# Kernel optimization log

Hardware: AMD Instinct MI355X
Metric: run time of the kernel (lower is better)

Reference implementation:

```python
import jax, jax.numpy as jnp
import numpy as np

B, L, D, H, W = 2, 4096, 1024, 16, 128
E = D // H

def _ln(x, g, b):
    m = jnp.mean(x, axis=-1, keepdims=True)
    v = jnp.mean((x - m) ** 2, axis=-1, keepdims=True)
    return (x - m) / jnp.sqrt(v + 1e-5) * g + b

def _swa(xn, Wqkv, bqkv, Wp, bp):
    # causal sliding-window attention: query i attends keys j in [i-W+1, i]
    b_, l_, d_ = xn.shape
    nb = l_ // W
    qkv = xn @ Wqkv + bqkv
    q, k, v = jnp.split(qkv, 3, axis=-1)
    def heads(t):
        return t.reshape(b_, l_, H, E).transpose(0, 2, 1, 3)  # [B,H,L,E]
    q, k, v = heads(q), heads(k), heads(v)
    def blk(t):
        return t.reshape(b_, H, nb, W, E)
    qb, kb, vb = blk(q), blk(k), blk(v)
    # each query block sees previous block + own block (covers the W-band)
    kprev = jnp.pad(kb, ((0, 0), (0, 0), (1, 0), (0, 0), (0, 0)))[:, :, :nb]
    vprev = jnp.pad(vb, ((0, 0), (0, 0), (1, 0), (0, 0), (0, 0)))[:, :, :nb]
    kc = jnp.concatenate([kprev, kb], axis=3)  # [B,H,nb,2W,E]
    vc = jnp.concatenate([vprev, vb], axis=3)
    scores = jnp.einsum('bhnre,bhnse->bhnrs', qb, kc) / np.float32(np.sqrt(E))
    r = jnp.arange(W)[:, None]
    s = jnp.arange(2 * W)[None, :]
    band = (s >= r + 1) & (s <= r + W)          # local coords of [i-W+1, i]
    first = band & (s >= W)                     # block 0 has no previous block
    mask = jnp.concatenate([first[None], jnp.broadcast_to(band, (nb - 1, W, 2 * W))], axis=0)
    scores = jnp.where(mask[None, None], scores, jnp.float32(-1e30))
    attn = jax.nn.softmax(scores, axis=-1)
    out = jnp.einsum('bhnrs,bhnse->bhnre', attn, vc)
    out = out.reshape(b_, H, l_, E).transpose(0, 2, 1, 3).reshape(b_, l_, d_)
    return out @ Wp + bp

def _linattn(xn, Wqkv, bqkv, Wo, bo):
    # chunked recurrent form of causal linear attention (same math as cumsum version)
    b_, l_, d_ = xn.shape
    C = 128
    nc = l_ // C
    qkv = xn @ Wqkv + bqkv
    q, k, v = jnp.split(qkv, 3, axis=-1)
    q = q.reshape(b_, l_, H, E)
    k = k.reshape(b_, l_, H, E)
    v = v.reshape(b_, l_, H, E)
    q = jax.nn.elu(q * np.float32(E ** -0.5)) + np.float32(1.0001)
    k = jax.nn.elu(k) + np.float32(1.0001)
    def chunks(t):
        return t.reshape(b_, nc, C, H, E).transpose(1, 0, 3, 2, 4)  # [nc,B,H,C,E]
    qc, kc, vc = chunks(q), chunks(k), chunks(v)
    tril = jnp.tril(jnp.ones((C, C), jnp.float32))
    def step(carry, inp):
        S, z = carry
        qi, ki, vi = inp
        A = jnp.einsum('bhce,bhde->bhcd', qi, ki) * tril
        num = jnp.einsum('bhce,bhef->bhcf', qi, S) + jnp.einsum('bhcd,bhdf->bhcf', A, vi)
        den = jnp.einsum('bhce,bhe->bhc', qi, z) + A.sum(-1)
        o = num / (den[..., None] + 1e-6)
        S = S + jnp.einsum('bhce,bhcf->bhef', ki, vi)
        z = z + ki.sum(2)
        return (S, z), o
    S0 = jnp.zeros((b_, H, E, E), jnp.float32)
    z0 = jnp.zeros((b_, H, E), jnp.float32)
    _, out = jax.lax.scan(step, (S0, z0), (qc, kc, vc))
    out = out.transpose(1, 0, 3, 2, 4).reshape(b_, l_, d_)
    return out @ Wo + bo

def setup_inputs() -> dict:
    key = jax.random.key(0)
    ks = jax.random.split(key, 9)
    def w(k, shape, s=0.02):
        return jax.random.normal(k, shape, jnp.float32) * s
    return {
        'x': jax.random.normal(ks[0], (B, L, D), jnp.float32),
        'g1': jnp.ones((D,), jnp.float32), 'b1': jnp.zeros((D,), jnp.float32),
        'Wqkv_a': w(ks[1], (D, 3 * D)), 'bqkv_a': jnp.zeros((3 * D,), jnp.float32),
        'Wp_a': w(ks[2], (D, D)), 'bp_a': jnp.zeros((D,), jnp.float32),
        'Wqkv_s': w(ks[3], (D, 3 * D)), 'bqkv_s': jnp.zeros((3 * D,), jnp.float32),
        'Wo_s': w(ks[4], (D, D)), 'bo_s': jnp.zeros((D,), jnp.float32),
        'Wo': w(ks[5], (D, D)), 'bo': jnp.zeros((D,), jnp.float32),
        'gm': jnp.ones((D,), jnp.float32), 'bm': jnp.zeros((D,), jnp.float32),
        'W1': w(ks[6], (D, 4 * D)), 'b1m': jnp.zeros((4 * D,), jnp.float32),
        'W2': w(ks[7], (4 * D, D)), 'b2m': jnp.zeros((D,), jnp.float32),
    }

def reference(x, g1, b1, Wqkv_a, bqkv_a, Wp_a, bp_a, Wqkv_s, bqkv_s, Wo_s, bo_s,
              Wo, bo, gm, bm, W1, b1m, W2, b2m):
    xn = _ln(x, g1, b1)
    attn_out = _swa(xn, Wqkv_a, bqkv_a, Wp_a, bp_a)
    ssm_out = _linattn(xn, Wqkv_s, bqkv_s, Wo_s, bo_s)
    mixed = (attn_out + ssm_out) @ Wo + bo
    x1 = x + mixed
    h = _ln(x1, gm, bm)
    mlp = jax.nn.gelu(h @ W1 + b1m, approximate=False) @ W2 + b2m
    return x1 + mlp
```

## Files before the change

kernel.cpp:

```cpp
#include <hip/hip_runtime.h>
#include <hip/hip_bf16.h>
#include <math.h>

typedef __hip_bfloat16 bf16;
typedef float f32x4 __attribute__((ext_vector_type(4)));
typedef short short8 __attribute__((ext_vector_type(8)));
typedef unsigned short u16x4 __attribute__((ext_vector_type(4)));
typedef unsigned short u16x8 __attribute__((ext_vector_type(8)));

#define AS1 __attribute__((address_space(1)))
#define AS3 __attribute__((address_space(3)))

__device__ __forceinline__ void gload16(const void* g, void* l) {
  __builtin_amdgcn_global_load_lds((const AS1 unsigned int*)g, (AS3 unsigned int*)l, 16, 0, 0);
}
__device__ __forceinline__ float b2f(unsigned short u) {
  union { unsigned int i; float f; } c; c.i = ((unsigned int)u) << 16; return c.f;
}
__device__ __forceinline__ unsigned short f2b(float f) {
  bf16 h = __float2bfloat16(f);
  unsigned short s; __builtin_memcpy(&s, &h, 2); return s;
}
__device__ __forceinline__ f32x4 mfma16(short8 a, short8 b, f32x4 c) {
  return __builtin_amdgcn_mfma_f32_16x16x32_bf16(a, b, c, 0, 0, 0);
// ... 31 lines not shown
    int N, int dld, int doff) {
  __shared__ __attribute__((aligned(16))) unsigned short t[64][72];
  const int k0 = blockIdx.x * 64, n0 = blockIdx.y * 64;
  const int tid = threadIdx.x;
#pragma unroll
  for (int i = 0; i < 2; ++i) {
    int c = i * 256 + tid;
    int row = c >> 3, c8 = c & 7;
    f32x4 a = *(const f32x4*)&S[(size_t)(k0 + row) * N + n0 + c8 * 8];
    f32x4 b = *(const f32x4*)&S[(size_t)(k0 + row) * N + n0 + c8 * 8 + 4];
    u16x8 o;
#pragma unroll
    for (int j = 0; j < 4; ++j) { o[j] = f2b(a[j]); o[4 + j] = f2b(b[j]); }
    *(u16x8*)&t[row][c8 * 8] = o;
  }
  __syncthreads();
#pragma unroll
  for (int i = 0; i < 2; ++i) {
    int c = i * 256 + tid;
    int nrow = c >> 3, k8 = c & 7;
    u16x8 o;
#pragma unroll
    for (int j = 0; j < 8; ++j) o[j] = t[k8 * 8 + j][nrow];
    *(u16x8*)&D[(size_t)(n0 + nrow) * dld + doff + k0 + k8 * 8] = o;
  }
}

__global__ __launch_bounds__(256) void bias_comb(
    const float* __restrict__ a, const float* __restrict__ b, float* __restrict__ o) {
  int i = blockIdx.x * 256 + threadIdx.x;
  o[i] = a[i] + b[i];
}

#define EPI_STORE 0
#define EPI_GELU 1
#define EPI_RES 2

template <int EPI, int OF32>
__global__ __launch_bounds__(256) void gemm_bt(
    const unsigned short* __restrict__ A, const unsigned short* __restrict__ Bt,
    const float* __restrict__ bias, void* __restrict__ Cv,
    const float* __restrict__ res, int K, int ldA, int ldC) {
  __shared__ __attribute__((aligned(16))) unsigned short As[128 * 32];
  __shared__ __attribute__((aligned(16))) unsigned short Bs[128 * 32];
  const int tid = threadIdx.x, lane = tid & 63, wv = tid >> 6;
  const int wr = wv >> 1, wc = wv & 1;
  const size_t arow0 = (size_t)blockIdx.x * 128;
  const size_t brow0 = (size_t)blockIdx.y * 128;
  const int g = lane >> 4, r = lane & 15;
  f32x4 acc[4][4] = {};
  const int nK = K >> 5;
  for (int kt = 0; kt < nK; ++kt) {
    const int k0 = kt << 5;
#pragma unroll
    for (int i = 0; i < 2; ++i) {
      int chunk = (wv * 2 + i) * 64 + lane;
      int row = chunk >> 2;
      int cc = (chunk & 3) ^ (row & 3);
      gload16(&A[(arow0 + row) * ldA + k0 + cc * 8], &As[(wv * 2 + i) * 512]);
      gload16(&Bt[(brow0 + row) * (size_t)K + k0 + cc * 8], &Bs[(wv * 2 + i) * 512]);
    }
    __syncthreads();
    short8 af[4], bfr[4];
#pragma unroll
    for (int m = 0; m < 4; ++m) {
      int row = wr * 64 + m * 16 + r;
      af[m] = *(const short8*)&As[row * 32 + ((g ^ (row & 3)) * 8)];
    }
#pragma unroll
    for (int n = 0; n < 4; ++n) {
      int row = wc * 64 + n * 16 + r;
      bfr[n] = *(const short8*)&Bs[row * 32 + ((g ^ (row & 3)) * 8)];
    }
#pragma unroll
    for (int m = 0; m < 4; ++m)
#pragma unroll
      for (int n = 0; n < 4; ++n)
        acc[m][n] = mfma16(af[m], bfr[n], acc[m][n]);
    __syncthreads();
  }
#pragma unroll
  for (int m = 0; m < 4; ++m) {
#pragma unroll
    for (int n = 0; n < 4; ++n) {
      const int col = (int)brow0 + wc * 64 + n * 16 + r;
      const float bv = bias[col];
#pragma unroll
      for (int i = 0; i < 4; ++i) {
        const size_t row = arow0 + wr * 64 + m * 16 + g * 4 + i;
        float v = acc[m][n][i] + bv;
        if (EPI == EPI_GELU) v = 0.5f * v * (1.f + erff(v * 0.70710678118f));
        if (EPI == EPI_RES) v += res[row * ldC + col];
        if (OF32) ((float*)Cv)[row * ldC + col] = v;
        else ((unsigned short*)Cv)[row * ldC + col] = f2b(v);
      }
    }
  }
}

__global__ __launch_bounds__(256) void swa_kernel(
    const unsigned short* __restrict__ qkv, unsigned short* __restrict__ outc) {
  __shared__ __attribute__((aligned(16))) unsigned short Ks[256 * 64];
  __shared__ __attribute__((aligned(16))) unsigned short Vt[64 * 264];
  __shared__ __attribute__((aligned(16))) unsigned short Ps[128 * 264];
  __shared__ __attribute__((aligned(16))) float dn[128];
  const int bid = blockIdx.x;
  const int qb = bid & 31, h = (bid >> 5) & 15, b = bid >> 9;
  const long btok = (long)b * 4096;
  const long tok0 = btok + (long)qb * 128;
  const int tid = threadIdx.x, lane = tid & 63, wv = tid >> 6;
  const int g = lane >> 4, r = lane & 15;

#pragma unroll
  for (int i = 0; i < 8; ++i) {
    int chunk = (wv * 8 + i) * 64 + lane;
    int s = chunk >> 3, cc = (chunk & 7) ^ (s & 7);
    long kt = tok0 - 128 + s; if (kt < btok) kt = btok;
    gload16(&qkv[(size_t)kt * 3072 + 1024 + h * 64 + cc * 8], &Ks[(wv * 8 + i) * 512]);
  }
#pragma unroll
  for (int i = 0; i < 8; ++i) {
    int chunk = i * 256 + tid;
    int s = chunk >> 3, e8 = chunk & 7;
    long kt = tok0 - 128 + s; if (kt < btok) kt = btok;
    u16x8 u = *(const u16x8*)&qkv[(size_t)kt * 3072 + 2048 + h * 64 + e8 * 8];
#pragma unroll
    for (int j = 0; j < 8; ++j) Vt[(e8 * 8 + j) * 264 + s] = u[j];
  }
  short8 qf[2][2];
#pragma unroll
  for (int m = 0; m < 2; ++m)
#pragma unroll
    for (int kc = 0; kc < 2; ++kc)
      qf[m][kc] = *(const short8*)&qkv[(size_t)(tok0 + wv * 32 + m * 16 + r) * 3072 + h * 64 + kc * 32 + g * 8];
  __syncthreads();

  float rs[2][4] = {};
  for (int n = 0; n < 16; ++n) {
    const int srow = n * 16 + r;
    short8 kf0 = *(const short8*)&Ks[srow * 64 + ((g) ^ (srow & 7)) * 8];
    short8 kf1 = *(const short8*)&Ks[srow * 64 + ((4 + g) ^ (srow & 7)) * 8];
#pragma unroll
    for (int m = 0; m < 2; ++m) {
      f32x4 acc = {0.f, 0.f, 0.f, 0.f};
      acc = mfma16(qf[m][0], kf0, acc);
      acc = mfma16(qf[m][1], kf1, acc);
#pragma unroll
      for (int i = 0; i < 4; ++i) {
        int rr = wv * 32 + m * 16 + g * 4 + i;
        int ss = n * 16 + r;
        bool valid = (ss >= rr + 1) && (ss <= rr + 128) && (qb > 0 || ss >= 128);
        float p = valid ? __expf(acc[i] * 0.125f) : 0.f;
        rs[m][i] += p;
        Ps[rr * 264 + ss] = f2b(p);
      }
    }
  }
#pragma unroll
  for (int m = 0; m < 2; ++m)
#pragma unroll
    for (int i = 0; i < 4; ++i) {
      float v = rs[m][i];
      v += __shfl_xor(v, 1); v += __shfl_xor(v, 2);
      v += __shfl_xor(v, 4); v += __shfl_xor(v, 8);
      if (r == i) dn[wv * 32 + m * 16 + g * 4 + i] = v;
    }
  __syncthreads();
// ... 10 lines not shown
#pragma unroll
    for (int m = 0; m < 2; ++m)
#pragma unroll
      for (int n = 0; n < 4; ++n)
        oacc[m][n] = mfma16(pf[m], vf[n], oacc[m][n]);
  }
#pragma unroll
  for (int m = 0; m < 2; ++m) {
    f32x4 dv = *(const f32x4*)&dn[wv * 32 + m * 16 + g * 4];
#pragma unroll
    for (int n = 0; n < 4; ++n) {
      int col = h * 64 + n * 16 + r;
#pragma unroll
      for (int i = 0; i < 4; ++i) {
        size_t row = (size_t)(tok0 + wv * 32 + m * 16 + g * 4 + i);
        outc[row * 2048 + col] = f2b(oacc[m][n][i] / dv[i]);
      }
    }
  }
}

__global__ __launch_bounds__(256) void lin_pass1(
    const unsigned short* __restrict__ qkv, float* __restrict__ KVt, float* __restrict__ kz) {
  __shared__ __attribute__((aligned(16))) unsigned short kf[128 * 72];
  __shared__ __attribute__((aligned(16))) unsigned short vs[128 * 72];
  const int bid = blockIdx.x;
  const int ch = bid & 31, h = (bid >> 5) & 15, b = bid >> 9;
  const size_t tok0 = (size_t)b * 4096 + (size_t)ch * 128;
  const int tid = threadIdx.x;
#pragma unroll
  for (int i = 0; i < 4; ++i) {
    int c = i * 256 + tid;
    int row = c >> 3, e8 = c & 7;
    u16x8 uk = *(const u16x8*)&qkv[(tok0 + row) * 3072 + 1024 + h * 64 + e8 * 8];
    u16x8 uv = *(const u16x8*)&qkv[(tok0 + row) * 3072 + 2048 + h * 64 + e8 * 8];
    u16x8 tk;
#pragma unroll
    for (int j = 0; j < 8; ++j) {
      float x = b2f(uk[j]);
      x = (x > 0.f) ? x : expm1f(x);
      tk[j] = f2b(x + 1.0001f);
    }
    *(u16x8*)&kf[row * 72 + e8 * 8] = tk;
    *(u16x8*)&vs[row * 72 + e8 * 8] = uv;
  }
  __syncthreads();
  const int e0 = (tid & 15) * 4, f0 = (tid >> 4) * 4;
  float acc[4][4] = {};
  for (int c = 0; c < 128; ++c) {
    u16x4 ku = *(const u16x4*)&kf[c * 72 + e0];
    u16x4 vu = *(const u16x4*)&vs[c * 72 + f0];
    float ke[4], vv[4];
#pragma unroll
    for (int j = 0; j < 4; ++j) { ke[j] = b2f(ku[j]); vv[j] = b2f(vu[j]); }
#pragma unroll
    for (int jf = 0; jf < 4; ++jf)
#pragma unroll
      for (int je = 0; je < 4; ++je)
        acc[jf][je] += vv[jf] * ke[je];
  }
  const size_t base = (size_t)bid * 4096;
#pragma unroll
  for (int jf = 0; jf < 4; ++jf) {
    f32x4 o = {acc[jf][0], acc[jf][1], acc[jf][2], acc[jf][3]};
    *(f32x4*)&KVt[base + (f0 + jf) * 64 + e0] = o;
  }
  if (tid < 64) {
    float s = 0.f;
// ... 15 lines not shown
      *(f32x4*)p = run[i];
      run[i] += c;
    }
  }
  if (tid < 64) {
    float rz = 0.f;
    for (int ch = 0; ch < 32; ++ch) {
      float* p = &kz[((size_t)bh * 32 + ch) * 64 + tid];
      float c = *p; *p = rz; rz += c;
    }
  }
}

__global__ __launch_bounds__(256) void lin_pass3(
    const unsigned short* __restrict__ qkv, const float* __restrict__ KVt,
    const float* __restrict__ kz, unsigned short* __restrict__ outc) {
  __shared__ __attribute__((aligned(16))) unsigned short qf[128 * 72];
  __shared__ __attribute__((aligned(16))) unsigned short kf[128 * 72];
  __shared__ __attribute__((aligned(16))) unsigned short vt[64 * 136];
  __shared__ __attribute__((aligned(16))) unsigned short st[64 * 72];
  __shared__ __attribute__((aligned(16))) unsigned short am[128 * 136];
  __shared__ __attribute__((aligned(16))) float zs[64];
  __shared__ __attribute__((aligned(16))) float dnl[128];
  const int bid = blockIdx.x;
  const int ch = bid & 31, h = (bid >> 5) & 15, b = bid >> 9;
  const size_t tok0 = (size_t)b * 4096 + (size_t)ch * 128;
  const int tid = threadIdx.x, lane = tid & 63, wv = tid >> 6;
  const int g = lane >> 4, r = lane & 15;

#pragma unroll
  for (int i = 0; i < 4; ++i) {
    int c = i * 256 + tid;
    int row = c >> 3, e8 = c & 7;
    u16x8 uq = *(const u16x8*)&qkv[(tok0 + row) * 3072 + h * 64 + e8 * 8];
    u16x8 uk = *(const u16x8*)&qkv[(tok0 + row) * 3072 + 1024 + h * 64 + e8 * 8];
    u16x8 uv = *(const u16x8*)&qkv[(tok0 + row) * 3072 + 2048 + h * 64 + e8 * 8];
    u16x8 tq, tk;
#pragma unroll
    for (int j = 0; j < 8; ++j) {
      float x = b2f(uq[j]) * 0.125f;
      x = (x > 0.f) ? x : expm1f(x);
      tq[j] = f2b(x + 1.0001f);
      float y = b2f(uk[j]);
      y = (y > 0.f) ? y : expm1f(y);
      tk[j] = f2b(y + 1.0001f);
    }
    *(u16x8*)&qf[row * 72 + e8 * 8] = tq;
    *(u16x8*)&kf[row * 72 + e8 * 8] = tk;
#pragma unroll
    for (int j = 0; j < 8; ++j) vt[(e8 * 8 + j) * 136 + row] = uv[j];
  }
#pragma unroll
  for (int i = 0; i < 2; ++i) {
    int idx = i * 256 + tid;
    int f = idx >> 3, e8 = idx & 7;
    f32x4 s0 = *(const f32x4*)&KVt[(size_t)bid * 4096 + f * 64 + e8 * 8];
    f32x4 s1 = *(const f32x4*)&KVt[(size_t)bid * 4096 + f * 64 + e8 * 8 + 4];
    u16x8 t;
#pragma unroll
    for (int j = 0; j < 4; ++j) { t[j] = f2b(s0[j]); t[4 + j] = f2b(s1[j]); }
    *(u16x8*)&st[f * 72 + e8 * 8] = t;
  }
  if (tid < 64) zs[tid] = kz[(size_t)bid * 64 + tid];
  __syncthreads();

  short8 aq[2][2];
#pragma unroll
  for (int m = 0; m < 2; ++m)
#pragma unroll
// ... 80 lines not shown
      }
    }
  }
}

extern "C" void kernel_launch(void* const* d_in, const int* in_sizes, int n_in,
                              void* d_out, int out_size, void* d_ws, size_t ws_size,
                              hipStream_t stream) {
  (void)in_sizes; (void)n_in; (void)out_size; (void)ws_size;
  const float* x      = (const float*)d_in[0];
  const float* g1     = (const float*)d_in[1];
  const float* b1     = (const float*)d_in[2];
  const float* Wqkv_a = (const float*)d_in[3];
  const float* bqkv_a = (const float*)d_in[4];
  const float* Wp_a   = (const float*)d_in[5];
  const float* bp_a   = (const float*)d_in[6];
  const float* Wqkv_s = (const float*)d_in[7];
  const float* bqkv_s = (const float*)d_in[8];
  const float* Wo_s   = (const float*)d_in[9];
  const float* bo_s   = (const float*)d_in[10];
  const float* Wo     = (const float*)d_in[11];
  const float* bo     = (const float*)d_in[12];
  const float* gm     = (const float*)d_in[13];
  const float* bm     = (const float*)d_in[14];
  const float* W1     = (const float*)d_in[15];
  const float* b1m    = (const float*)d_in[16];
  const float* W2     = (const float*)d_in[17];
  const float* b2m    = (const float*)d_in[18];
  float* out = (float*)d_out;

  char* ws = (char*)d_ws;
  size_t off = 0;
  auto alloc = [&](size_t bytes) { char* p = ws + off; off += (bytes + 255) & ~(size_t)255; return p; };
  unsigned short* wTa   = (unsigned short*)alloc((size_t)3072 * 1024 * 2);
  unsigned short* wTs   = (unsigned short*)alloc((size_t)3072 * 1024 * 2);
  unsigned short* wTpo  = (unsigned short*)alloc((size_t)1024 * 2048 * 2);
  unsigned short* wTo   = (unsigned short*)alloc((size_t)1024 * 1024 * 2);
  unsigned short* wT1   = (unsigned short*)alloc((size_t)4096 * 1024 * 2);
  unsigned short* wT2   = (unsigned short*)alloc((size_t)1024 * 4096 * 2);
  float*          bcomb = (float*)alloc(1024 * 4);
  unsigned short* xn    = (unsigned short*)alloc((size_t)8192 * 1024 * 2);
  unsigned short* qkvA  = (unsigned short*)alloc((size_t)8192 * 3072 * 2);
  unsigned short* qkvS  = (unsigned short*)alloc((size_t)8192 * 3072 * 2);
  unsigned short* comb  = (unsigned short*)alloc((size_t)8192 * 2048 * 2);
  float*          kvt   = (float*)alloc((size_t)1024 * 4096 * 4);
  float*          kzp   = (float*)alloc((size_t)1024 * 64 * 4);
  unsigned short* gbuf  = qkvA;
  unsigned short* sum   = (unsigned short*)kvt;
  unsigned short* h_    = xn;
  float*          x1    = (float*)comb;

  transpose_w<<<dim3(16, 48), 256, 0, stream>>>(Wqkv_a, wTa, 3072, 1024, 0);
  transpose_w<<<dim3(16, 48), 256, 0, stream>>>(Wqkv_s, wTs, 3072, 1024, 0);
  transpose_w<<<dim3(16, 16), 256, 0, stream>>>(Wp_a, wTpo, 1024, 2048, 0);
  transpose_w<<<dim3(16, 16), 256, 0, stream>>>(Wo_s, wTpo, 1024, 2048, 1024);
  transpose_w<<<dim3(16, 16), 256, 0, stream>>>(Wo, wTo, 1024, 1024, 0);
  transpose_w<<<dim3(16, 64), 256, 0, stream>>>(W1, wT1, 4096, 1024, 0);
  transpose_w<<<dim3(64, 16), 256, 0, stream>>>(W2, wT2, 1024, 4096, 0);
  bias_comb<<<4, 256, 0, stream>>>(bp_a, bo_s, bcomb);

  ln_kernel<<<8192, 256, 0, stream>>>(x, g1, b1, xn);
  gemm_bt<EPI_STORE, 0><<<dim3(64, 24), 256, 0, stream>>>(xn, wTa, bqkv_a, qkvA, nullptr, 1024, 1024, 3072);
  swa_kernel<<<1024, 256, 0, stream>>>(qkvA, comb);
  gemm_bt<EPI_STORE, 0><<<dim3(64, 24), 256, 0, stream>>>(xn, wTs, bqkv_s, qkvS, nullptr, 1024, 1024, 3072);
  lin_pass1<<<1024, 256, 0, stream>>>(qkvS, kvt, kzp);
  lin_pass2<<<32, 256, 0, stream>>>(kvt, kzp);
  lin_pass3<<<1024, 256, 0, stream>>>(qkvS, kvt, kzp, comb);
  gemm_bt<EPI_STORE, 0><<<dim3(64, 8), 256, 0, stream>>>(comb, wTpo, bcomb, sum, nullptr, 2048, 2048, 1024);
  gemm_bt<EPI_RES, 1><<<dim3(64, 8), 256, 0, stream>>>(sum, wTo, bo, x1, x, 1024, 1024, 1024);
  ln_kernel<<<8192, 256, 0, stream>>>(x1, gm, bm, h_);
  gemm_bt<EPI_GELU, 0><<<dim3(64, 32), 256, 0, stream>>>(h_, wT1, b1m, gbuf, nullptr, 1024, 1024, 4096);
  gemm_bt<EPI_RES, 1><<<dim3(64, 8), 256, 0, stream>>>(gbuf, wT2, b2m, out, x1, 4096, 4096, 1024);
}
```

Baseline: 649.2 us.

## Replace GEMM with 512-thread 256-wide tiles and 4-stage pipelined global-to-LDS loads

Replaces the 128x128 single-stage GEMM with a 512-thread kernel using 256x256 or 128x256 tiles and a 4-buffer LDS ring that prefetches two K-steps ahead via direct global-to-LDS loads with explicit vmcnt waits. It adds workgroup swizzling for L2 locality and s_setprio around MFMA bursts. The aim is to hide global load latency, remove the per-iteration double __syncthreads stall and raise arithmetic intensity per tile. Larger tiles mean fewer workgroups and more LDS per block, which may limit occupancy. The per-wave LDS addressing drops the old XOR swizzle, so correctness depends on the new load mapping lining up with the fragment reads.

```diff
diff --git a/kernel.cpp b/kernel.cpp
--- a/kernel.cpp
+++ b/kernel.cpp
@@ -91,58 +91,113 @@
 #define EPI_GELU 1
 #define EPI_RES 2
 
-template <int EPI, int OF32>
-__global__ __launch_bounds__(256) void gemm_bt(
+
+#define MMQ(Q)                                                                     \
+  do {                                                                             \
+    _Pragma("unroll") for (int mm_ = 0; mm_ < 4; ++mm_) {                          \
+      _Pragma("unroll") for (int nn_ = 0; nn_ < 4; ++nn_)                          \
+          acc[(Q) * 4 + mm_][nn_] = mfma16(af[mm_], bf[nn_], acc[(Q) * 4 + mm_][nn_]); \
+    }                                                                              \
+  } while (0)
+
+#define SLOT(RR, RRS, S_)                                                          \
+  do {                                                                             \
+    const int s2_ = (S_) + 2;                                                      \
+    const bool st_ = s2_ < nS;                                                     \
+    short8 af[4], bf[4];                                                           \
+    _Pragma("unroll") for (int f_ = 0; f_ < 4; ++f_)                               \
+        af[f_] = *(const short8*)&Abuf[RR][awo + f_ * 512];                         \
+    _Pragma("unroll") for (int f_ = 0; f_ < 4; ++f_)                               \
+        bf[f_] = *(const short8*)&Bbuf[RR][bwo + f_ * 512];                         \
+    if (st_) {                                                                     \
+      gload16(gA + (size_t)s2_ * 32, &Abuf[RRS][wv * 512]);                        \
+      if constexpr (MSUB == 8) {                                                   \
+        gload16(gA + (size_t)s2_ * 32 + 128 * ldAs, &Abuf[RRS][(8 + wv) * 512]);   \
+      } else {                                                                     \
+        gload16(gB + (size_t)s2_ * 32, &Bbuf[RRS][wv * 512]);                      \
+        gload16(gB + (size_t)s2_ * 32 + 128 * Ksz, &Bbuf[RRS][(8 + wv) * 512]);    \
+      }                                                                            \
+    }                                                                              \
+    __builtin_amdgcn_s_barrier();                                                  \
+    __builtin_amdgcn_s_setprio(1);                                                 \
+    MMQ(0);                                                                        \
+    __builtin_amdgcn_s_setprio(0);                                                 \
+    if constexpr (MSUB == 8) {                                                     \
+      __builtin_amdgcn_s_barrier();                                                \
+      _Pragma("unroll") for (int f_ = 0; f_ < 4; ++f_)                             \
+          af[f_] = *(const short8*)&Abuf[RR][awo + (4 + f_) * 512];                 \
+      if (st_) {                                                                   \
+        gload16(gB + (size_t)s2_ * 32, &Bbuf[RRS][wv * 512]);                      \
+        gload16(gB + (size_t)s2_ * 32 + 128 * Ksz, &Bbuf[RRS][(8 + wv) * 512]);    \
+      }                                                                            \
+      __builtin_amdgcn_s_barrier();                                                \
+      __builtin_amdgcn_s_setprio(1);                                               \
+      MMQ(1);                                                                      \
+      __builtin_amdgcn_s_setprio(0);                                               \
+    }                                                                              \
+    if (st_) {                                                                     \
+      if constexpr (MSUB == 8) asm volatile("s_waitcnt vmcnt(4)" ::: "memory");    \
+      else asm volatile("s_waitcnt vmcnt(3)" ::: "memory");                        \
+    } else if ((S_) + 1 < nS) {                                                    \
+      asm volatile("s_waitcnt vmcnt(0)" ::: "memory");                             \
+    }                                                                              \
+    __builtin_amdgcn_s_barrier();                                                  \
+    __builtin_amdgcn_sched_barrier(0);                                             \
+  } while (0)
+
+template <int MSUB, int EPI, int OF32>
+__global__ __launch_bounds__(512, 2) void gemm8(
     const unsigned short* __restrict__ A, const unsigned short* __restrict__ Bt,
     const float* __restrict__ bias, void* __restrict__ Cv,
-    const float* __restrict__ res, int K, int ldA, int ldC) {
-  __shared__ __attribute__((aligned(16))) unsigned short As[128 * 32];
-  __shared__ __attribute__((aligned(16))) unsigned short Bs[128 * 32];
+    const float* __restrict__ res, int K, int ldA, int ldC, int lgnmt) {
+  static_assert(MSUB == 8 || MSUB == 4, "MSUB must be 8 (BM=256) or 4 (BM=128)");
+  __shared__ __attribute__((aligned(16))) unsigned short Abuf[4][MSUB * 1024];
+  __shared__ __attribute__((aligned(16))) unsigned short Bbuf[4][8192];
   const int tid = threadIdx.x, lane = tid & 63, wv = tid >> 6;
-  const int wr = wv >> 1, wc = wv & 1;
-  const size_t arow0 = (size_t)blockIdx.x * 128;
-  const size_t brow0 = (size_t)blockIdx.y * 128;
   const int g = lane >> 4, r = lane & 15;
-  f32x4 acc[4][4] = {};
-  const int nK = K >> 5;
-  for (int kt = 0; kt < nK; ++kt) {
-    const int k0 = kt << 5;
-#pragma unroll
-    for (int i = 0; i < 2; ++i) {
-      int chunk = (wv * 2 + i) * 64 + lane;
-      int row = chunk >> 2;
-      int cc = (chunk & 3) ^ (row & 3);
-      gload16(&A[(arow0 + row) * ldA + k0 + cc * 8], &As[(wv * 2 + i) * 512]);
-      gload16(&Bt[(brow0 + row) * (size_t)K + k0 + cc * 8], &Bs[(wv * 2 + i) * 512]);
-    }
-    __syncthreads();
-    short8 af[4], bfr[4];
-#pragma unroll
-    for (int m = 0; m < 4; ++m) {
-      int row = wr * 64 + m * 16 + r;
-      af[m] = *(const short8*)&As[row * 32 + ((g ^ (row & 3)) * 8)];
-    }
-#pragma unroll
-    for (int n = 0; n < 4; ++n) {
-      int row = wc * 64 + n * 16 + r;
-      bfr[n] = *(const short8*)&Bs[row * 32 + ((g ^ (row & 3)) * 8)];
-    }
-#pragma unroll
-    for (int m = 0; m < 4; ++m)
-#pragma unroll
-      for (int n = 0; n < 4; ++n)
-        acc[m][n] = mfma16(af[m], bfr[n], acc[m][n]);
-    __syncthreads();
-  }
-#pragma unroll
-  for (int m = 0; m < 4; ++m) {
+  const int wr = wv >> 2, wc = wv & 3;
+  const int bid = blockIdx.x, nwg = gridDim.x;
+  const int swz = (bid & 7) * (nwg >> 3) + (bid >> 3);
+  const int mt = swz & ((1 << lgnmt) - 1), nt = swz >> lgnmt;
+  const size_t arow0 = (size_t)mt * (MSUB * 32);
+  const size_t brow0 = (size_t)nt * 256;
+  const size_t Ksz = (size_t)K, ldAs = (size_t)ldA;
+  const unsigned short* gA = A + (arow0 + (size_t)(wv * 16 + r)) * ldAs + g * 8;
+  const unsigned short* gB = Bt + (brow0 + (size_t)(wv * 16 + r)) * Ksz + g * 8;
+  const int awo = wr * (MSUB * 512) + lane * 8;
+  const int bwo = wc * 2048 + lane * 8;
+  const int nS = K >> 5;
+  f32x4 acc[MSUB][4] = {};
+
+  gload16(gA, &Abuf[0][wv * 512]);
+  if constexpr (MSUB == 8) gload16(gA + 128 * ldAs, &Abuf[0][(8 + wv) * 512]);
+  gload16(gB, &Bbuf[0][wv * 512]);
+  gload16(gB + 128 * Ksz, &Bbuf[0][(8 + wv) * 512]);
+  gload16(gA + 32, &Abuf[1][wv * 512]);
+  if constexpr (MSUB == 8) gload16(gA + 32 + 128 * ldAs, &Abuf[1][(8 + wv) * 512]);
+  gload16(gB + 32, &Bbuf[1][wv * 512]);
+  gload16(gB + 32 + 128 * Ksz, &Bbuf[1][(8 + wv) * 512]);
+  if constexpr (MSUB == 8) asm volatile("s_waitcnt vmcnt(4)" ::: "memory");
+  else                     asm volatile("s_waitcnt vmcnt(3)" ::: "memory");
+  __builtin_amdgcn_s_barrier();
+  __builtin_amdgcn_sched_barrier(0);
+
+  for (int s4 = 0; s4 < nS; s4 += 4) {
+    SLOT(0, 2, s4 + 0);
+    SLOT(1, 3, s4 + 1);
+    SLOT(2, 0, s4 + 2);
+    SLOT(3, 1, s4 + 3);
+  }
+
+#pragma unroll
+  for (int m = 0; m < MSUB; ++m) {
 #pragma unroll
     for (int n = 0; n < 4; ++n) {
       const int col = (int)brow0 + wc * 64 + n * 16 + r;
       const float bv = bias[col];
 #pragma unroll
       for (int i = 0; i < 4; ++i) {
-        const size_t row = arow0 + wr * 64 + m * 16 + g * 4 + i;
+        const size_t row = arow0 + wr * (MSUB * 16) + m * 16 + g * 4 + i;
         float v = acc[m][n][i] + bv;
         if (EPI == EPI_GELU) v = 0.5f * v * (1.f + erff(v * 0.70710678118f));
         if (EPI == EPI_RES) v += res[row * ldC + col];
@@ -524,15 +579,15 @@
   bias_comb<<<4, 256, 0, stream>>>(bp_a, bo_s, bcomb);
 
   ln_kernel<<<8192, 256, 0, stream>>>(x, g1, b1, xn);
-  gemm_bt<EPI_STORE, 0><<<dim3(64, 24), 256, 0, stream>>>(xn, wTa, bqkv_a, qkvA, nullptr, 1024, 1024, 3072);
+  gemm8<8, EPI_STORE, 0><<<384, 512, 0, stream>>>(xn, wTa, bqkv_a, qkvA, nullptr, 1024, 1024, 3072, 5);
   swa_kernel<<<1024, 256, 0, stream>>>(qkvA, comb);
-  gemm_bt<EPI_STORE, 0><<<dim3(64, 24), 256, 0, stream>>>(xn, wTs, bqkv_s, qkvS, nullptr, 1024, 1024, 3072);
+  gemm8<8, EPI_STORE, 0><<<384, 512, 0, stream>>>(xn, wTs, bqkv_s, qkvS, nullptr, 1024, 1024, 3072, 5);
   lin_pass1<<<1024, 256, 0, stream>>>(qkvS, kvt, kzp);
   lin_pass2<<<32, 256, 0, stream>>>(kvt, kzp);
   lin_pass3<<<1024, 256, 0, stream>>>(qkvS, kvt, kzp, comb);
-  gemm_bt<EPI_STORE, 0><<<dim3(64, 8), 256, 0, stream>>>(comb, wTpo, bcomb, sum, nullptr, 2048, 2048, 1024);
-  gemm_bt<EPI_RES, 1><<<dim3(64, 8), 256, 0, stream>>>(sum, wTo, bo, x1, x, 1024, 1024, 1024);
+  gemm8<4, EPI_STORE, 0><<<256, 512, 0, stream>>>(comb, wTpo, bcomb, sum, nullptr, 2048, 2048, 1024, 6);
+  gemm8<4, EPI_RES, 1><<<256, 512, 0, stream>>>(sum, wTo, bo, x1, x, 1024, 1024, 1024, 6);
   ln_kernel<<<8192, 256, 0, stream>>>(x1, gm, bm, h_);
-  gemm_bt<EPI_GELU, 0><<<dim3(64, 32), 256, 0, stream>>>(h_, wT1, b1m, gbuf, nullptr, 1024, 1024, 4096);
-  gemm_bt<EPI_RES, 1><<<dim3(64, 8), 256, 0, stream>>>(gbuf, wT2, b2m, out, x1, 4096, 4096, 1024);
-}
+  gemm8<8, EPI_GELU, 0><<<512, 512, 0, stream>>>(h_, wT1, b1m, gbuf, nullptr, 1024, 1024, 4096, 5);
+  gemm8<4, EPI_RES, 1><<<256, 512, 0, stream>>>(gbuf, wT2, b2m, out, x1, 4096, 4096, 1024, 6);
+}
```

New measurement: 699.1 us. +7.7%, slower.

## Replace GEMM with 8-wave double-buffered ping-pong kernel using larger tiles

Applied to the files above, without the earlier changes.

Replaces the simple 128x128, K=32 single-buffered GEMM with a 512-thread kernel. It uses 256x256 (or 256x128) tiles, K=64 steps and double-buffered LDS. Global-to-LDS loads are interleaved with MFMA phases, using explicit barriers, s_setprio and vmcnt waits. A grid swizzle improves L2 locality. The aim is to hide memory latency and raise MFMA utilization across all the dense projections. The risks are higher LDS and register use, fragile hand-written synchronization, and fewer blocks for the smaller GEMMs.

```diff
diff --git a/kernel.cpp b/kernel.cpp
--- a/kernel.cpp
+++ b/kernel.cpp
@@ -91,67 +91,145 @@
 #define EPI_GELU 1
 #define EPI_RES 2
 
-template <int EPI, int OF32>
-__global__ __launch_bounds__(256) void gemm_bt(
+
+#define BAR() asm volatile("s_barrier" ::: "memory")
+#define PRIO1 __builtin_amdgcn_s_setprio(1)
+#define PRIO0 __builtin_amdgcn_s_setprio(0)
+#define VM2 asm volatile("s_waitcnt vmcnt(2)" ::: "memory")
+#define VM0 asm volatile("s_waitcnt vmcnt(0)" ::: "memory")
+
+#define RDA(CUR, MH)                                                                 \
+  _Pragma("unroll") for (int m_ = 0; m_ < 4; ++m_)                                   \
+  _Pragma("unroll") for (int ks_ = 0; ks_ < 2; ++ks_)                                \
+    a[m_][ks_] = *(const short8*)&Abuf[CUR][((wr * 8 + (MH) * 4 + m_) + 16 * ks_) * 512 + lane * 8];
+
+#define RDB(CUR, NH, BB)                                                             \
+  _Pragma("unroll") for (int n_ = 0; n_ < NQ; ++n_)                                  \
+  _Pragma("unroll") for (int ks_ = 0; ks_ < 2; ++ks_) {                              \
+    if constexpr (NQ == 2)                                                           \
+      BB[n_][ks_] = *(const short8*)&Bbuf[CUR][((wc * 4 + (NH) * 2 + n_) + 16 * ks_) * 512 + lane * 8]; \
+    else                                                                             \
+      BB[n_][ks_] = *(const short8*)&Bbuf[CUR][((wc * 2 + (NH)) + 8 * ks_) * 512 + lane * 8]; \
+  }
+
+#define MMPH(MH, NH, BB)                                                             \
+  _Pragma("unroll") for (int m_ = 0; m_ < 4; ++m_)                                   \
+  _Pragma("unroll") for (int n_ = 0; n_ < NQ; ++n_)                                  \
+  _Pragma("unroll") for (int ks_ = 0; ks_ < 2; ++ks_)                                \
+    acc[MH][NH][m_][n_] = mfma16(a[m_][ks_], BB[n_][ks_], acc[MH][NH][m_][n_]);
+
+#define STA_LO(DST, T_) do { const unsigned short* p_ = pA0 + (size_t)(T_) * 64;     \
+    gload16(p_, &Abuf[DST][wv * 512]);                                               \
+    gload16(p_ + 128 * ldAs, &Abuf[DST][(8 + wv) * 512]); } while (0)
+#define STA_HI(DST, T_) do { const unsigned short* p_ = pA0 + (size_t)(T_) * 64 + 32;\
+    gload16(p_, &Abuf[DST][(16 + wv) * 512]);                                        \
+    gload16(p_ + 128 * ldAs, &Abuf[DST][(24 + wv) * 512]); } while (0)
+#define STB_0(DST, T_) do { const unsigned short* p_ = pB0 + (size_t)(T_) * 64;      \
+    if constexpr (NQ == 2) {                                                         \
+      gload16(p_, &Bbuf[DST][wv * 512]);                                             \
+      gload16(p_ + 128 * Ksz, &Bbuf[DST][(8 + wv) * 512]);                           \
+    } else {                                                                         \
+      gload16(p_, &Bbuf[DST][wv * 512]);                                             \
+      gload16(p_ + 32, &Bbuf[DST][(8 + wv) * 512]);                                  \
+    } } while (0)
+#define STB_1(DST, T_) do { if constexpr (NQ == 2) {                                 \
+      const unsigned short* p_ = pB0 + (size_t)(T_) * 64 + 32;                       \
+      gload16(p_, &Bbuf[DST][(16 + wv) * 512]);                                      \
+      gload16(p_ + 128 * Ksz, &Bbuf[DST][(24 + wv) * 512]); } } while (0)
+
+#define TILE(CUR, T_)                                                                \
+  do {                                                                               \
+    const int Tp1_ = (T_) + 1, Tp2_ = (T_) + 2;                                      \
+    const bool s1_ = Tp1_ < nT, s2_ = Tp2_ < nT;                                     \
+                                            \
+    RDA(CUR, 0); RDB(CUR, 0, b0);                                                    \
+    if (s1_) STA_HI(CUR ^ 1, Tp1_);                                                  \
+    BAR(); PRIO1; MMPH(0, 0, b0); PRIO0; BAR();                                      \
+                                                   \
+    RDB(CUR, 1, b1);                                                                 \
+    if (s1_) STB_0(CUR ^ 1, Tp1_);                                                   \
+    BAR(); PRIO1; MMPH(0, 1, b1); PRIO0; BAR();                                      \
+                                                   \
+    RDA(CUR, 1);                                                                     \
+    if (s1_) STB_1(CUR ^ 1, Tp1_);                                                   \
+    BAR(); PRIO1; MMPH(1, 0, b0); PRIO0; BAR();                                      \
+                  \
+    if (s2_) STA_LO(CUR, Tp2_);                                                      \
+    BAR(); PRIO1; MMPH(1, 1, b1); PRIO0;                                             \
+    if (s2_) { VM2; } else { VM0; }                                                  \
+    BAR();                                                                           \
+  } while (0)
+
+template <int NQ, int EPI, int OF32>
+__global__ __launch_bounds__(512, 2) void gemm8p(
     const unsigned short* __restrict__ A, const unsigned short* __restrict__ Bt,
     const float* __restrict__ bias, void* __restrict__ Cv,
-    const float* __restrict__ res, int K, int ldA, int ldC) {
-  __shared__ __attribute__((aligned(16))) unsigned short As[128 * 32];
-  __shared__ __attribute__((aligned(16))) unsigned short Bs[128 * 32];
+    const float* __restrict__ res, int K, int ldA, int ldC, int lgnmt) {
+  __shared__ __attribute__((aligned(16))) unsigned short Abuf[2][256 * 64];
+  __shared__ __attribute__((aligned(16))) unsigned short Bbuf[2][NQ * 128 * 64];
   const int tid = threadIdx.x, lane = tid & 63, wv = tid >> 6;
-  const int wr = wv >> 1, wc = wv & 1;
-  const size_t arow0 = (size_t)blockIdx.x * 128;
-  const size_t brow0 = (size_t)blockIdx.y * 128;
   const int g = lane >> 4, r = lane & 15;
-  f32x4 acc[4][4] = {};
-  const int nK = K >> 5;
-  for (int kt = 0; kt < nK; ++kt) {
-    const int k0 = kt << 5;
-#pragma unroll
-    for (int i = 0; i < 2; ++i) {
-      int chunk = (wv * 2 + i) * 64 + lane;
-      int row = chunk >> 2;
-      int cc = (chunk & 3) ^ (row & 3);
-      gload16(&A[(arow0 + row) * ldA + k0 + cc * 8], &As[(wv * 2 + i) * 512]);
-      gload16(&Bt[(brow0 + row) * (size_t)K + k0 + cc * 8], &Bs[(wv * 2 + i) * 512]);
-    }
-    __syncthreads();
-    short8 af[4], bfr[4];
+  const int wr = wv >> 2, wc = wv & 3;
+  const int bid = blockIdx.x, nwg = gridDim.x;
+  const int swz = (bid & 7) * (nwg >> 3) + (bid >> 3);
+  const int mt = swz & ((1 << lgnmt) - 1), nt = swz >> lgnmt;
+  const size_t arow0 = (size_t)mt * 256;
+  const size_t brow0 = (size_t)nt * (NQ * 128);
+  const size_t ldAs = (size_t)ldA, Ksz = (size_t)K;
+  const unsigned short* pA0 = A + (arow0 + (size_t)(wv * 16 + r)) * ldAs + g * 8;
+  const unsigned short* pB0 = Bt + (brow0 + (size_t)(wv * 16 + r)) * Ksz + g * 8;
+  const int nT = K >> 6;
+  short8 a[4][2], b0[NQ][2], b1[NQ][2];
+  f32x4 acc[2][2][4][NQ] = {};
+
+  STA_LO(0, 0); STA_HI(0, 0); STB_0(0, 0); STB_1(0, 0);
+  STA_LO(1, 1);
+  VM2;
+  BAR();
+
+  for (int T = 0; T < nT; T += 2) {
+    TILE(0, T);
+    TILE(1, T + 1);
+  }
+
+#pragma unroll
+  for (int mh = 0; mh < 2; ++mh) {
 #pragma unroll
     for (int m = 0; m < 4; ++m) {
-      int row = wr * 64 + m * 16 + r;
-      af[m] = *(const short8*)&As[row * 32 + ((g ^ (row & 3)) * 8)];
-    }
-#pragma unroll
-    for (int n = 0; n < 4; ++n) {
-      int row = wc * 64 + n * 16 + r;
-      bfr[n] = *(const short8*)&Bs[row * 32 + ((g ^ (row & 3)) * 8)];
-    }
-#pragma unroll
-    for (int m = 0; m < 4; ++m)
-#pragma unroll
-      for (int n = 0; n < 4; ++n)
-        acc[m][n] = mfma16(af[m], bfr[n], acc[m][n]);
-    __syncthreads();
-  }
-#pragma unroll
-  for (int m = 0; m < 4; ++m) {
-#pragma unroll
-    for (int n = 0; n < 4; ++n) {
-      const int col = (int)brow0 + wc * 64 + n * 16 + r;
-      const float bv = bias[col];
-#pragma unroll
-      for (int i = 0; i < 4; ++i) {
-        const size_t row = arow0 + wr * 64 + m * 16 + g * 4 + i;
-        float v = acc[m][n][i] + bv;
-        if (EPI == EPI_GELU) v = 0.5f * v * (1.f + erff(v * 0.70710678118f));
-        if (EPI == EPI_RES) v += res[row * ldC + col];
-        if (OF32) ((float*)Cv)[row * ldC + col] = v;
-        else ((unsigned short*)Cv)[row * ldC + col] = f2b(v);
+#pragma unroll
+      for (int nh = 0; nh < 2; ++nh) {
+#pragma unroll
+        for (int n = 0; n < NQ; ++n) {
+          const int col = (int)brow0 + wc * (32 * NQ) + nh * (16 * NQ) + n * 16 + r;
+          const float bv = bias[col];
+#pragma unroll
+          for (int i = 0; i < 4; ++i) {
+            const size_t row = arow0 + wr * 128 + mh * 64 + m * 16 + g * 4 + i;
+            float v = acc[mh][nh][m][n][i] + bv;
+            if (EPI == EPI_GELU) v = 0.5f * v * (1.f + erff(v * 0.70710678118f));
+            if (EPI == EPI_RES) v += res[row * ldC + col];
+            if (OF32) ((float*)Cv)[row * ldC + col] = v;
+            else ((unsigned short*)Cv)[row * ldC + col] = f2b(v);
+          }
+        }
       }
     }
   }
 }
+
+#undef TILE
+#undef STA_LO
+#undef STA_HI
+#undef STB_0
+#undef STB_1
+#undef RDA
+#undef RDB
+#undef MMPH
+#undef BAR
+#undef PRIO1
+#undef PRIO0
+#undef VM2
+#undef VM0
 
 __global__ __launch_bounds__(256) void swa_kernel(
     const unsigned short* __restrict__ qkv, unsigned short* __restrict__ outc) {
@@ -524,15 +602,15 @@
   bias_comb<<<4, 256, 0, stream>>>(bp_a, bo_s, bcomb);
 
   ln_kernel<<<8192, 256, 0, stream>>>(x, g1, b1, xn);
-  gemm_bt<EPI_STORE, 0><<<dim3(64, 24), 256, 0, stream>>>(xn, wTa, bqkv_a, qkvA, nullptr, 1024, 1024, 3072);
+  gemm8p<2, EPI_STORE, 0><<<384, 512, 0, stream>>>(xn, wTa, bqkv_a, qkvA, nullptr, 1024, 1024, 3072, 5);
   swa_kernel<<<1024, 256, 0, stream>>>(qkvA, comb);
-  gemm_bt<EPI_STORE, 0><<<dim3(64, 24), 256, 0, stream>>>(xn, wTs, bqkv_s, qkvS, nullptr, 1024, 1024, 3072);
+  gemm8p<2, EPI_STORE, 0><<<384, 512, 0, stream>>>(xn, wTs, bqkv_s, qkvS, nullptr, 1024, 1024, 3072, 5);
   lin_pass1<<<1024, 256, 0, stream>>>(qkvS, kvt, kzp);
   lin_pass2<<<32, 256, 0, stream>>>(kvt, kzp);
   lin_pass3<<<1024, 256, 0, stream>>>(qkvS, kvt, kzp, comb);
-  gemm_bt<EPI_STORE, 0><<<dim3(64, 8), 256, 0, stream>>>(comb, wTpo, bcomb, sum, nullptr, 2048, 2048, 1024);
-  gemm_bt<EPI_RES, 1><<<dim3(64, 8), 256, 0, stream>>>(sum, wTo, bo, x1, x, 1024, 1024, 1024);
+  gemm8p<1, EPI_STORE, 0><<<256, 512, 0, stream>>>(comb, wTpo, bcomb, sum, nullptr, 2048, 2048, 1024, 5);
+  gemm8p<1, EPI_RES, 1><<<256, 512, 0, stream>>>(sum, wTo, bo, x1, x, 1024, 1024, 1024, 5);
   ln_kernel<<<8192, 256, 0, stream>>>(x1, gm, bm, h_);
-  gemm_bt<EPI_GELU, 0><<<dim3(64, 32), 256, 0, stream>>>(h_, wT1, b1m, gbuf, nullptr, 1024, 1024, 4096);
-  gemm_bt<EPI_RES, 1><<<dim3(64, 8), 256, 0, stream>>>(gbuf, wT2, b2m, out, x1, 4096, 4096, 1024);
-}
+  gemm8p<2, EPI_GELU, 0><<<512, 512, 0, stream>>>(h_, wT1, b1m, gbuf, nullptr, 1024, 1024, 4096, 5);
+  gemm8p<1, EPI_RES, 1><<<256, 512, 0, stream>>>(gbuf, wT2, b2m, out, x1, 4096, 4096, 1024, 5);
+}
```

Result: slower. 753.4 us (+16.1%).

## Double-buffer GEMM with larger tiles and merge both QKV projections

Applied to the files above, without the earlier changes.

Replaces the single-buffered 128x128 GEMM with a 512-thread double-buffered kernel that prefetches the next K-slice while running MFMAs on the current one. It uses 128x256 or 64x256 tiles, a swizzled block order for L2 reuse, and raises priority around the MFMA loop. The two QKV projections are fused into a single N=6144 GEMM with a concatenated bias and interleaved output, and all downstream readers are updated to the new row stride. Registers per thread go up, and the LDS layout drops the XOR swizzle, so bank conflicts are a risk.

```diff
diff --git a/kernel.cpp b/kernel.cpp
--- a/kernel.cpp
+++ b/kernel.cpp
@@ -87,62 +87,81 @@
   o[i] = a[i] + b[i];
 }
 
+__global__ __launch_bounds__(256) void bias_cat(
+    const float* __restrict__ a, const float* __restrict__ b, float* __restrict__ o, int N) {
+  int i = blockIdx.x * 256 + threadIdx.x;
+  o[i] = (i < N) ? a[i] : b[i - N];
+}
+
 #define EPI_STORE 0
 #define EPI_GELU 1
 #define EPI_RES 2
 
-template <int EPI, int OF32>
-__global__ __launch_bounds__(256) void gemm_bt(
+template <int TM, int EPI, int OF32>
+__global__ __launch_bounds__(512, 4) void gemm2p(
     const unsigned short* __restrict__ A, const unsigned short* __restrict__ Bt,
     const float* __restrict__ bias, void* __restrict__ Cv,
-    const float* __restrict__ res, int K, int ldA, int ldC) {
-  __shared__ __attribute__((aligned(16))) unsigned short As[128 * 32];
-  __shared__ __attribute__((aligned(16))) unsigned short Bs[128 * 32];
+    const float* __restrict__ res, int K, int ldA, int ldC, int lgnmt) {
+  __shared__ __attribute__((aligned(16))) unsigned short Ab[2][TM * 4 * 512];
+  __shared__ __attribute__((aligned(16))) unsigned short Bb[2][16 * 512];
   const int tid = threadIdx.x, lane = tid & 63, wv = tid >> 6;
-  const int wr = wv >> 1, wc = wv & 1;
-  const size_t arow0 = (size_t)blockIdx.x * 128;
-  const size_t brow0 = (size_t)blockIdx.y * 128;
   const int g = lane >> 4, r = lane & 15;
-  f32x4 acc[4][4] = {};
-  const int nK = K >> 5;
-  for (int kt = 0; kt < nK; ++kt) {
-    const int k0 = kt << 5;
-#pragma unroll
-    for (int i = 0; i < 2; ++i) {
-      int chunk = (wv * 2 + i) * 64 + lane;
-      int row = chunk >> 2;
-      int cc = (chunk & 3) ^ (row & 3);
-      gload16(&A[(arow0 + row) * ldA + k0 + cc * 8], &As[(wv * 2 + i) * 512]);
-      gload16(&Bt[(brow0 + row) * (size_t)K + k0 + cc * 8], &Bs[(wv * 2 + i) * 512]);
-    }
-    __syncthreads();
-    short8 af[4], bfr[4];
-#pragma unroll
-    for (int m = 0; m < 4; ++m) {
-      int row = wr * 64 + m * 16 + r;
-      af[m] = *(const short8*)&As[row * 32 + ((g ^ (row & 3)) * 8)];
-    }
-#pragma unroll
-    for (int n = 0; n < 4; ++n) {
-      int row = wc * 64 + n * 16 + r;
-      bfr[n] = *(const short8*)&Bs[row * 32 + ((g ^ (row & 3)) * 8)];
-    }
-#pragma unroll
-    for (int m = 0; m < 4; ++m)
+  const int wr = wv >> 2, wc = wv & 3;
+  const int bid = blockIdx.x, nwg = gridDim.x;
+  const int swz = (bid & 7) * (nwg >> 3) + (bid >> 3);
+  const int mt = swz & ((1 << lgnmt) - 1), nt = swz >> lgnmt;
+  const size_t arow0 = (size_t)mt * (TM * 64);
+  const size_t brow0 = (size_t)nt * 256;
+  const size_t ldAs = (size_t)ldA, Ksz = (size_t)K;
+  const int aw = wv & (TM * 4 - 1);
+  const unsigned short* gA = A + (arow0 + (size_t)(aw * 16 + r)) * ldAs + g * 8;
+  const unsigned short* gB0 = Bt + (brow0 + (size_t)(wv * 16 + r)) * Ksz + g * 8;
+  const unsigned short* gB1 = gB0 + 128 * Ksz;
+  const int nS = K >> 5;
+  f32x4 acc[TM * 2][4] = {};
+
+  if (TM == 2 || wv < 4) gload16(gA, &Ab[0][aw * 512]);
+  gload16(gB0, &Bb[0][wv * 512]);
+  gload16(gB1, &Bb[0][(8 + wv) * 512]);
+  asm volatile("s_waitcnt vmcnt(0)" ::: "memory");
+  __builtin_amdgcn_s_barrier();
+
+  for (int s = 0; s < nS; ++s) {
+    const int cur = s & 1;
+    if (s + 1 < nS) {
+      const size_t ko = (size_t)(s + 1) * 32;
+      if (TM == 2 || wv < 4) gload16(gA + ko, &Ab[cur ^ 1][aw * 512]);
+      gload16(gB0 + ko, &Bb[cur ^ 1][wv * 512]);
+      gload16(gB1 + ko, &Bb[cur ^ 1][(8 + wv) * 512]);
+    }
+    short8 af[TM * 2], bfr[4];
+#pragma unroll
+    for (int m = 0; m < TM * 2; ++m)
+      af[m] = *(const short8*)&Ab[cur][(wr * (TM * 2) + m) * 512 + lane * 8];
+#pragma unroll
+    for (int n = 0; n < 4; ++n)
+      bfr[n] = *(const short8*)&Bb[cur][(wc * 4 + n) * 512 + lane * 8];
+    __builtin_amdgcn_s_setprio(1);
+#pragma unroll
+    for (int m = 0; m < TM * 2; ++m)
 #pragma unroll
       for (int n = 0; n < 4; ++n)
         acc[m][n] = mfma16(af[m], bfr[n], acc[m][n]);
-    __syncthreads();
-  }
-#pragma unroll
-  for (int m = 0; m < 4; ++m) {
+    __builtin_amdgcn_s_setprio(0);
+    asm volatile("s_waitcnt vmcnt(0)" ::: "memory");
+    __builtin_amdgcn_s_barrier();
+    __builtin_amdgcn_sched_barrier(0);
+  }
+
+#pragma unroll
+  for (int m = 0; m < TM * 2; ++m) {
 #pragma unroll
     for (int n = 0; n < 4; ++n) {
       const int col = (int)brow0 + wc * 64 + n * 16 + r;
       const float bv = bias[col];
 #pragma unroll
       for (int i = 0; i < 4; ++i) {
-        const size_t row = arow0 + wr * 64 + m * 16 + g * 4 + i;
+        const size_t row = arow0 + wr * (TM * 32) + m * 16 + g * 4 + i;
         float v = acc[m][n][i] + bv;
         if (EPI == EPI_GELU) v = 0.5f * v * (1.f + erff(v * 0.70710678118f));
         if (EPI == EPI_RES) v += res[row * ldC + col];
@@ -171,14 +190,14 @@
     int chunk = (wv * 8 + i) * 64 + lane;
     int s = chunk >> 3, cc = (chunk & 7) ^ (s & 7);
     long kt = tok0 - 128 + s; if (kt < btok) kt = btok;
-    gload16(&qkv[(size_t)kt * 3072 + 1024 + h * 64 + cc * 8], &Ks[(wv * 8 + i) * 512]);
+    gload16(&qkv[(size_t)kt * 6144 + 1024 + h * 64 + cc * 8], &Ks[(wv * 8 + i) * 512]);
   }
 #pragma unroll
   for (int i = 0; i < 8; ++i) {
     int chunk = i * 256 + tid;
     int s = chunk >> 3, e8 = chunk & 7;
     long kt = tok0 - 128 + s; if (kt < btok) kt = btok;
-    u16x8 u = *(const u16x8*)&qkv[(size_t)kt * 3072 + 2048 + h * 64 + e8 * 8];
+    u16x8 u = *(const u16x8*)&qkv[(size_t)kt * 6144 + 2048 + h * 64 + e8 * 8];
 #pragma unroll
     for (int j = 0; j < 8; ++j) Vt[(e8 * 8 + j) * 264 + s] = u[j];
   }
@@ -187,7 +206,7 @@
   for (int m = 0; m < 2; ++m)
 #pragma unroll
     for (int kc = 0; kc < 2; ++kc)
-      qf[m][kc] = *(const short8*)&qkv[(size_t)(tok0 + wv * 32 + m * 16 + r) * 3072 + h * 64 + kc * 32 + g * 8];
+      qf[m][kc] = *(const short8*)&qkv[(size_t)(tok0 + wv * 32 + m * 16 + r) * 6144 + h * 64 + kc * 32 + g * 8];
   __syncthreads();
 
   float rs[2][4] = {};
@@ -264,8 +283,8 @@
   for (int i = 0; i < 4; ++i) {
     int c = i * 256 + tid;
     int row = c >> 3, e8 = c & 7;
-    u16x8 uk = *(const u16x8*)&qkv[(tok0 + row) * 3072 + 1024 + h * 64 + e8 * 8];
-    u16x8 uv = *(const u16x8*)&qkv[(tok0 + row) * 3072 + 2048 + h * 64 + e8 * 8];
+    u16x8 uk = *(const u16x8*)&qkv[(tok0 + row) * 6144 + 1024 + h * 64 + e8 * 8];
+    u16x8 uv = *(const u16x8*)&qkv[(tok0 + row) * 6144 + 2048 + h * 64 + e8 * 8];
     u16x8 tk;
 #pragma unroll
     for (int j = 0; j < 8; ++j) {
@@ -347,9 +366,9 @@
   for (int i = 0; i < 4; ++i) {
     int c = i * 256 + tid;
     int row = c >> 3, e8 = c & 7;
-    u16x8 uq = *(const u16x8*)&qkv[(tok0 + row) * 3072 + h * 64 + e8 * 8];
-    u16x8 uk = *(const u16x8*)&qkv[(tok0 + row) * 3072 + 1024 + h * 64 + e8 * 8];
-    u16x8 uv = *(const u16x8*)&qkv[(tok0 + row) * 3072 + 2048 + h * 64 + e8 * 8];
+    u16x8 uq = *(const u16x8*)&qkv[(tok0 + row) * 6144 + h * 64 + e8 * 8];
+    u16x8 uk = *(const u16x8*)&qkv[(tok0 + row) * 6144 + 1024 + h * 64 + e8 * 8];
+    u16x8 uv = *(const u16x8*)&qkv[(tok0 + row) * 6144 + 2048 + h * 64 + e8 * 8];
     u16x8 tq, tk;
 #pragma unroll
     for (int j = 0; j < 8; ++j) {
@@ -496,43 +515,42 @@
   char* ws = (char*)d_ws;
   size_t off = 0;
   auto alloc = [&](size_t bytes) { char* p = ws + off; off += (bytes + 255) & ~(size_t)255; return p; };
-  unsigned short* wTa   = (unsigned short*)alloc((size_t)3072 * 1024 * 2);
-  unsigned short* wTs   = (unsigned short*)alloc((size_t)3072 * 1024 * 2);
+  unsigned short* wTaS  = (unsigned short*)alloc((size_t)6144 * 1024 * 2);
   unsigned short* wTpo  = (unsigned short*)alloc((size_t)1024 * 2048 * 2);
   unsigned short* wTo   = (unsigned short*)alloc((size_t)1024 * 1024 * 2);
   unsigned short* wT1   = (unsigned short*)alloc((size_t)4096 * 1024 * 2);
   unsigned short* wT2   = (unsigned short*)alloc((size_t)1024 * 4096 * 2);
   float*          bcomb = (float*)alloc(1024 * 4);
+  float*          bcat  = (float*)alloc(6144 * 4);
   unsigned short* xn    = (unsigned short*)alloc((size_t)8192 * 1024 * 2);
-  unsigned short* qkvA  = (unsigned short*)alloc((size_t)8192 * 3072 * 2);
-  unsigned short* qkvS  = (unsigned short*)alloc((size_t)8192 * 3072 * 2);
+  unsigned short* qkvAS = (unsigned short*)alloc((size_t)8192 * 6144 * 2);
   unsigned short* comb  = (unsigned short*)alloc((size_t)8192 * 2048 * 2);
   float*          kvt   = (float*)alloc((size_t)1024 * 4096 * 4);
   float*          kzp   = (float*)alloc((size_t)1024 * 64 * 4);
-  unsigned short* gbuf  = qkvA;
+  unsigned short* gbuf  = qkvAS;
   unsigned short* sum   = (unsigned short*)kvt;
   unsigned short* h_    = xn;
   float*          x1    = (float*)comb;
 
-  transpose_w<<<dim3(16, 48), 256, 0, stream>>>(Wqkv_a, wTa, 3072, 1024, 0);
-  transpose_w<<<dim3(16, 48), 256, 0, stream>>>(Wqkv_s, wTs, 3072, 1024, 0);
+  transpose_w<<<dim3(16, 48), 256, 0, stream>>>(Wqkv_a, wTaS, 3072, 1024, 0);
+  transpose_w<<<dim3(16, 48), 256, 0, stream>>>(Wqkv_s, wTaS + (size_t)3072 * 1024, 3072, 1024, 0);
   transpose_w<<<dim3(16, 16), 256, 0, stream>>>(Wp_a, wTpo, 1024, 2048, 0);
   transpose_w<<<dim3(16, 16), 256, 0, stream>>>(Wo_s, wTpo, 1024, 2048, 1024);
   transpose_w<<<dim3(16, 16), 256, 0, stream>>>(Wo, wTo, 1024, 1024, 0);
   transpose_w<<<dim3(16, 64), 256, 0, stream>>>(W1, wT1, 4096, 1024, 0);
   transpose_w<<<dim3(64, 16), 256, 0, stream>>>(W2, wT2, 1024, 4096, 0);
   bias_comb<<<4, 256, 0, stream>>>(bp_a, bo_s, bcomb);
+  bias_cat<<<24, 256, 0, stream>>>(bqkv_a, bqkv_s, bcat, 3072);
 
   ln_kernel<<<8192, 256, 0, stream>>>(x, g1, b1, xn);
-  gemm_bt<EPI_STORE, 0><<<dim3(64, 24), 256, 0, stream>>>(xn, wTa, bqkv_a, qkvA, nullptr, 1024, 1024, 3072);
-  swa_kernel<<<1024, 256, 0, stream>>>(qkvA, comb);
-  gemm_bt<EPI_STORE, 0><<<dim3(64, 24), 256, 0, stream>>>(xn, wTs, bqkv_s, qkvS, nullptr, 1024, 1024, 3072);
-  lin_pass1<<<1024, 256, 0, stream>>>(qkvS, kvt, kzp);
+  gemm2p<2, EPI_STORE, 0><<<1536, 512, 0, stream>>>(xn, wTaS, bcat, qkvAS, nullptr, 1024, 1024, 6144, 6);
+  swa_kernel<<<1024, 256, 0, stream>>>(qkvAS, comb);
+  lin_pass1<<<1024, 256, 0, stream>>>(qkvAS + 3072, kvt, kzp);
   lin_pass2<<<32, 256, 0, stream>>>(kvt, kzp);
-  lin_pass3<<<1024, 256, 0, stream>>>(qkvS, kvt, kzp, comb);
-  gemm_bt<EPI_STORE, 0><<<dim3(64, 8), 256, 0, stream>>>(comb, wTpo, bcomb, sum, nullptr, 2048, 2048, 1024);
-  gemm_bt<EPI_RES, 1><<<dim3(64, 8), 256, 0, stream>>>(sum, wTo, bo, x1, x, 1024, 1024, 1024);
+  lin_pass3<<<1024, 256, 0, stream>>>(qkvAS + 3072, kvt, kzp, comb);
+  gemm2p<1, EPI_STORE, 0><<<512, 512, 0, stream>>>(comb, wTpo, bcomb, sum, nullptr, 2048, 2048, 1024, 7);
+  gemm2p<1, EPI_RES, 1><<<512, 512, 0, stream>>>(sum, wTo, bo, x1, x, 1024, 1024, 1024, 7);
   ln_kernel<<<8192, 256, 0, stream>>>(x1, gm, bm, h_);
-  gemm_bt<EPI_GELU, 0><<<dim3(64, 32), 256, 0, stream>>>(h_, wT1, b1m, gbuf, nullptr, 1024, 1024, 4096);
-  gemm_bt<EPI_RES, 1><<<dim3(64, 8), 256, 0, stream>>>(gbuf, wT2, b2m, out, x1, 4096, 4096, 1024);
-}
+  gemm2p<2, EPI_GELU, 0><<<1024, 512, 0, stream>>>(h_, wT1, b1m, gbuf, nullptr, 1024, 1024, 4096, 6);
+  gemm2p<1, EPI_RES, 1><<<512, 512, 0, stream>>>(gbuf, wT2, b2m, out, x1, 4096, 4096, 1024, 7);
+}
```

After: 777.2 us. 19.7% more time.
